# Kernel optimization log

Hardware: AMD Instinct MI355X
Metric: run time of the kernel (lower is better)

## Reference

```python
import jax, jax.numpy as jnp
import numpy as np

L, B, T, V, E, H = 6, 4, 1024, 32000, 768, 12
D = E // H  # head_size = 64


def setup_inputs() -> dict:
    key = jax.random.key(0)
    ks = jax.random.split(key, 12)
    s = 0.02
    n = lambda k, shape: jax.random.normal(k, shape, jnp.float32) * s
    return {
        "idx": jax.random.randint(ks[0], (B, T), 0, V),
        "tok_emb": n(ks[1], (V, E)),
        "pos_emb": n(ks[2], (T, E)),
        "ln1_w": jnp.ones((L, E)), "ln1_b": jnp.zeros((L, E)),
        "wq": n(ks[3], (L, E, H, D)),
        "wk": n(ks[4], (L, E, H, D)),
        "wv": n(ks[5], (L, E, H, D)),
        "wo": n(ks[6], (L, E, E)), "bo": jnp.zeros((L, E)),
        "ln2_w": jnp.ones((L, E)), "ln2_b": jnp.zeros((L, E)),
        "w1": n(ks[7], (L, E, 4 * E)), "b1": jnp.zeros((L, 4 * E)),
        "w2": n(ks[8], (L, 4 * E, E)), "b2": jnp.zeros((L, E)),
        "lnf_w": jnp.ones((E,)), "lnf_b": jnp.zeros((E,)),
        "head_w": n(ks[9], (E, V)), "head_b": jnp.zeros((V,)),
    }


def _ln(x, w, b, eps=1e-5):
    m = x.mean(-1, keepdims=True)
    v = ((x - m) ** 2).mean(-1, keepdims=True)
    return (x - m) * jax.lax.rsqrt(v + eps) * w + b


def _forward(idx, tok_emb, pos_emb, ln1_w, ln1_b, wq, wk, wv, wo, bo,
             ln2_w, ln2_b, w1, b1, w2, b2, lnf_w, lnf_b, head_w, head_b):
    t = idx.shape[1]
    x = tok_emb[idx] + pos_emb[None, :t]          # [B,T,E]
    causal = jnp.tril(jnp.ones((t, t), bool))     # tril buffer
    scale = jnp.asarray(D, x.dtype) ** -0.5       # k.shape[-1] ** -0.5

    def block(x, p):
        l1w, l1b, Wq, Wk, Wv, Wo, Bo, l2w, l2b, W1, B1, W2, B2 = p
        h = _ln(x, l1w, l1b)
        q = jnp.einsum('btc,chd->bthd', h, Wq)
        k = jnp.einsum('btc,chd->bthd', h, Wk)
        v = jnp.einsum('btc,chd->bthd', h, Wv)
        wei = jnp.einsum('bqhd,bkhd->bhqk', q, k) * scale
        wei = jnp.where(causal, wei, -jnp.inf)
        wei = jax.nn.softmax(wei, axis=-1)
        att = jnp.einsum('bhqk,bkhd->bqhd', wei, v).reshape(x.shape)
        x = x + (att @ Wo + Bo)
        h2 = _ln(x, l2w, l2b)
        x = x + (jax.nn.relu(h2 @ W1 + B1) @ W2 + B2)
        return x, None

    params = (ln1_w, ln1_b, wq, wk, wv, wo, bo, ln2_w, ln2_b, w1, b1, w2, b2)
    x, _ = jax.lax.scan(block, x, params)
    x = _ln(x, lnf_w, lnf_b)
    return x @ head_w + head_b                    # [B,T,V] logits


def reference(idx, tok_emb, pos_emb, ln1_w, ln1_b, wq, wk, wv, wo, bo,
              ln2_w, ln2_b, w1, b1, w2, b2, lnf_w, lnf_b, head_w, head_b):
    return _forward(idx, tok_emb, pos_emb, ln1_w, ln1_b, wq, wk, wv, wo, bo,
                    ln2_w, ln2_b, w1, b1, w2, b2, lnf_w, lnf_b, head_w, head_b)
```

## Files before the change

### kernel.cpp

```cpp
#include <hip/hip_runtime.h>
#include <hip/hip_bf16.h>
#include <math.h>

#define L_LAYERS 6
#define BB 4
#define TT 1024
#define VV 32000
#define EE 768
#define HH 12
#define DD 64
#define BT (BB * TT)

typedef unsigned short u16;
typedef unsigned int   u32;
typedef __attribute__((ext_vector_type(8))) short short8;
typedef __attribute__((ext_vector_type(8))) unsigned short ushort8v;
typedef __attribute__((ext_vector_type(4))) float f32x4;

__device__ __forceinline__ float b2f_lo(u32 u) { union { u32 i; float f; } c; c.i = u << 16;          return c.f; }
__device__ __forceinline__ float b2f_hi(u32 u) { union { u32 i; float f; } c; c.i = u & 0xffff0000u;  return c.f; }
__device__ __forceinline__ u16  f2b(float f)   { union { float f; u32 i; } c{f}; u32 r = c.i + 0x7fffu + ((c.i >> 16) & 1u); return (u16)(r >> 16); }

__device__ __forceinline__ void gload16(const void* g, void* l) {
    __builtin_amdgcn_global_load_lds(
        (const __attribute__((address_space(1))) void*)g,
        (__attribute__((address_space(3))) void*)l, 16, 0, 0);
}

__global__ __launch_bounds__(256) void embed_kernel(
    const int* __restrict__ idx, const float* __restrict__ tok_emb,
    const float* __restrict__ pos_emb, float* __restrict__ x)
{
    int i = blockIdx.x * 256 + threadIdx.x;
    int e  = i % EE;
    int bt = i / EE;
    int t  = bt % TT;
    int tok = idx[bt];
    x[i] = tok_emb[(size_t)tok * EE + e] + pos_emb[(size_t)t * EE + e];
}

__global__ __launch_bounds__(256) void ln_kernel(
    const float* __restrict__ X, const float* __restrict__ w,
    const float* __restrict__ b, u16* __restrict__ Y)
{
    const int tid = threadIdx.x;
    const size_t row = blockIdx.x;
    const float* x = X + row * EE;

    float v0 = x[tid], v1 = x[tid + 256], v2 = x[tid + 512];

    __shared__ float red[256];
    red[tid] = v0 + v1 + v2;
    __syncthreads();
    for (int off = 128; off > 0; off >>= 1) {
        if (tid < off) red[tid] += red[tid + off];
        __syncthreads();
    }
    float mean = red[0] * (1.0f / EE);
    __syncthreads();
    float d0 = v0 - mean, d1 = v1 - mean, d2 = v2 - mean;
    red[tid] = d0 * d0 + d1 * d1 + d2 * d2;
    __syncthreads();
    for (int off = 128; off > 0; off >>= 1) {
        if (tid < off) red[tid] += red[tid + off];
        __syncthreads();
    }
    float rstd = rsqrtf(red[0] * (1.0f / EE) + 1e-5f);

    u16* y = Y + row * EE;
    y[tid]       = f2b(d0 * rstd * w[tid]       + b[tid]);
    y[tid + 256] = f2b(d1 * rstd * w[tid + 256] + b[tid + 256]);
    y[tid + 512] = f2b(d2 * rstd * w[tid + 512] + b[tid + 512]);
}

__device__ __forceinline__ void transpose_tile(
    const float* __restrict__ W, u16* __restrict__ Wt,
    int K, int N, int kt, int nt)
{
    __shared__ float t[32][33];
    const int k0 = kt * 32;
    const int n0 = nt * 32;
    const int c = threadIdx.x & 31;
    const int r = threadIdx.x >> 5;
    #pragma unroll
    for (int i = 0; i < 4; i++)
        t[r + i * 8][c] = W[(size_t)(k0 + r + i * 8) * N + n0 + c];
    __syncthreads();
    #pragma unroll
    for (int i = 0; i < 4; i++) {
        int rr = r + i * 8;
        Wt[(size_t)(n0 + rr) * K + k0 + c] = f2b(t[c][rr]);
    }
}

__global__ __launch_bounds__(256) void transpose_cvt(
    const float* __restrict__ W, u16* __restrict__ Wt, int K, int N)
{
    transpose_tile(W, Wt, K, N, blockIdx.y, blockIdx.x);
}

__global__ __launch_bounds__(256) void transpose_layer(
    const float* __restrict__ wq, const float* __restrict__ wk,
    const float* __restrict__ wv, const float* __restrict__ wo,
    const float* __restrict__ w1, const float* __restrict__ w2,
    u16* __restrict__ wt)
{
    const int t = blockIdx.x;
    if (t < 2304) {
        const int m = t / 576, r = t % 576;
        const float* Ws[4] = {wq, wk, wv, wo};
        transpose_tile(Ws[m], wt + (size_t)m * 768 * 768, 768, 768, r / 24, r % 24);
    } else if (t < 4608) {
        const int r = t - 2304;
        transpose_tile(w1, wt + (size_t)4 * 768 * 768, 768, 3072, r / 96, r % 96);
    } else {
        const int r = t - 4608;
        transpose_tile(w2, wt + (size_t)4 * 768 * 768 + (size_t)3072 * 768,
                       3072, 768, r / 24, r % 24);
    }
}

template<int RELU, int RES, int OUTBF, int MFRAG>
__global__ __launch_bounds__(256) void gemm_bf16(
    const u16* __restrict__ A,
    const u16* __restrict__ Bt,
    const float* __restrict__ bias,
    const float* __restrict__ res,
    void* __restrict__ Cv,
    int M, int N, int K)
{
    constexpr int TM = MFRAG * 32;
    __shared__ u16 As[TM * 64];
    __shared__ u16 Bs[128 * 64];

    const int tid  = threadIdx.x;
    const int lane = tid & 63;
    const int w    = tid >> 6;
    const int wr   = w >> 1, wc = w & 1;
    const int m0 = blockIdx.x * TM;
    const int n0 = blockIdx.y * 128;

    const int cs = (lane & 7) ^ (lane >> 3);
    const int rl = lane >> 3;

    int aoff[2 * MFRAG], boff[8];
    const int kq = lane >> 4;
    #pragma unroll
    for (int mi = 0; mi < MFRAG; mi++) {
        int rg = wr * (MFRAG * 16) + mi * 16 + (lane & 15);
        #pragma unroll
        for (int ks = 0; ks < 2; ks++)
            aoff[2 * mi + ks] = rg * 64 + (((ks * 4 + kq) ^ (rg & 7)) * 8);
    }
    #pragma unroll
    for (int ni = 0; ni < 4; ni++) {
        int rg = wc * 64 + ni * 16 + (lane & 15);
        #pragma unroll
        for (int ks = 0; ks < 2; ks++)
            boff[2 * ni + ks] = rg * 64 + (((ks * 4 + kq) ^ (rg & 7)) * 8);
    }

    f32x4 acc[MFRAG][4] = {};

    for (int k0 = 0; k0 < K; k0 += 64) {
        __syncthreads();
        #pragma unroll
        for (int i = 0; i < MFRAG; i++) {
            const int seg = i * 4 + w;
            const int row = seg * 8 + rl;
            gload16(A + (size_t)(m0 + row) * K + k0 + cs * 8, &As[seg * 512]);
        }
        #pragma unroll
        for (int i = 0; i < 4; i++) {
            const int seg = i * 4 + w;
            const int row = seg * 8 + rl;
            gload16(Bt + (size_t)(n0 + row) * K + k0 + cs * 8, &Bs[seg * 512]);
        }
        __syncthreads();
        #pragma unroll
        for (int ks = 0; ks < 2; ks++) {
            short8 af[MFRAG], bfv[4];
            #pragma unroll
            for (int mi = 0; mi < MFRAG; mi++) af[mi] = *(const short8*)&As[aoff[2 * mi + ks]];
            #pragma unroll
            for (int ni = 0; ni < 4; ni++) bfv[ni] = *(const short8*)&Bs[boff[2 * ni + ks]];
            #pragma unroll
            for (int mi = 0; mi < MFRAG; mi++)
                #pragma unroll
                for (int ni = 0; ni < 4; ni++)
                    acc[mi][ni] = __builtin_amdgcn_mfma_f32_16x16x32_bf16(
                        af[mi], bfv[ni], acc[mi][ni], 0, 0, 0);
        }
    }

    const int rbase = m0 + wr * (MFRAG * 16) + (lane >> 4) * 4;
    const int cbase = n0 + wc * 64 + (lane & 15);
    #pragma unroll
    for (int ni = 0; ni < 4; ni++) {
        const int c = cbase + ni * 16;
        const float bv = bias ? bias[c] : 0.0f;
        #pragma unroll
        for (int mi = 0; mi < MFRAG; mi++) {
            const int r = rbase + mi * 16;
            #pragma unroll
            for (int i = 0; i < 4; i++) {
                float v = acc[mi][ni][i] + bv;
                const size_t off = (size_t)(r + i) * N + c;
                if (RES)  v += res[off];
                if (RELU) v = fmaxf(v, 0.0f);
                if (OUTBF) ((u16*)Cv)[off] = f2b(v);
                else       ((float*)Cv)[off] = v;
            }
        }
    }
}

#define AST 76
__global__ __launch_bounds__(256) void attn_mfma(
    const u16* __restrict__ qkv, u16* __restrict__ O)
{
    const int tid = threadIdx.x;
    const int qi = blockIdx.x;
    const int h  = blockIdx.y;
    const int b  = blockIdx.z;
    const int q0 = qi * 64;

    __shared__ u16 Ks[64 * AST];
    __shared__ u16 Vt[64 * AST];
    __shared__ u16 Ps[64 * AST];

    const int lane = tid & 63;
    const int w    = tid >> 6;
    const int lr   = lane & 15;
    const int lk   = lane >> 4;

    const int sr = tid >> 2;
    const int sc = tid & 3;

    {
        const u16* src = qkv + (size_t)(b * TT + q0 + sr) * 2304 + h * 64 + sc * 16;
        *(ushort8v*)&Ps[sr * AST + sc * 16]     = *(const ushort8v*)src;
        *(ushort8v*)&Ps[sr * AST + sc * 16 + 8] = *(const ushort8v*)(src + 8);
    }
    __syncthreads();
    short8 aq[2];
    #pragma unroll
    for (int ks = 0; ks < 2; ks++)
        aq[ks] = *(const short8*)&Ps[(w * 16 + lr) * AST + lk * 8 + ks * 32];

    f32x4 oacc[4] = {};
    float m_run[4], l_run[4];
    #pragma unroll
    for (int i = 0; i < 4; i++) { m_run[i] = -3.0e38f; l_run[i] = 0.0f; }

    const int qrow = q0 + w * 16 + lk * 4;
    const int ntile = qi + 1;

    for (int t = 0; t < ntile; t++) {
        const int k0 = t * 64;
        __syncthreads();
        {
            const u16* ksrc = qkv + (size_t)(b * TT + k0 + sr) * 2304 + 768 + h * 64 + sc * 16;
            *(ushort8v*)&Ks[sr * AST + sc * 16]     = *(const ushort8v*)ksrc;
            *(ushort8v*)&Ks[sr * AST + sc * 16 + 8] = *(const ushort8v*)(ksrc + 8);
            const u16* vsrc = ksrc + 768;
            ushort8v v0 = *(const ushort8v*)vsrc;
            ushort8v v1 = *(const ushort8v*)(vsrc + 8);
            #pragma unroll
            for (int j = 0; j < 8; j++) Vt[(sc * 16 + j) * AST + sr]     = v0[j];
            #pragma unroll
            for (int j = 0; j < 8; j++) Vt[(sc * 16 + 8 + j) * AST + sr] = v1[j];
        }
        __syncthreads();

        f32x4 sfrag[4] = {};
        #pragma unroll
        for (int ks = 0; ks < 2; ks++)
            #pragma unroll
            for (int nt = 0; nt < 4; nt++) {
                short8 bk = *(const short8*)&Ks[(nt * 16 + lr) * AST + lk * 8 + ks * 32];
                sfrag[nt] = __builtin_amdgcn_mfma_f32_16x16x32_bf16(aq[ks], bk, sfrag[nt], 0, 0, 0);
            }

        float sv[4][4];
        #pragma unroll
        for (int i = 0; i < 4; i++) {
            float mx = -3.0e38f;
            #pragma unroll
            for (int nt = 0; nt < 4; nt++) {
                float s = sfrag[nt][i] * 0.125f;
                if (t == qi && (k0 + nt * 16 + lr) > (qrow + i)) s = -3.0e38f;
                sv[i][nt] = s;
                mx = fmaxf(mx, s);
            }
            mx = fmaxf(mx, __shfl_xor(mx, 1));
            mx = fmaxf(mx, __shfl_xor(mx, 2));
            mx = fmaxf(mx, __shfl_xor(mx, 4));
            mx = fmaxf(mx, __shfl_xor(mx, 8));
            const float m_new = fmaxf(m_run[i], mx);
            const float scale = __expf(m_run[i] - m_new);
            float rs = 0.0f;
            #pragma unroll
            for (int nt = 0; nt < 4; nt++) {
                float p = __expf(sv[i][nt] - m_new);
                sv[i][nt] = p;
                rs += p;
            }
            rs += __shfl_xor(rs, 1);
            rs += __shfl_xor(rs, 2);
            rs += __shfl_xor(rs, 4);
            rs += __shfl_xor(rs, 8);
            l_run[i] = l_run[i] * scale + rs;
            m_run[i] = m_new;
            #pragma unroll
            for (int dt = 0; dt < 4; dt++) oacc[dt][i] *= scale;
        }

        #pragma unroll
        for (int i = 0; i < 4; i++)
            #pragma unroll
            for (int nt = 0; nt < 4; nt++)
                Ps[(w * 16 + lk * 4 + i) * AST + nt * 16 + lr] = f2b(sv[i][nt]);
        __syncthreads();

        #pragma unroll
        for (int ks = 0; ks < 2; ks++) {
            short8 ap = *(const short8*)&Ps[(w * 16 + lr) * AST + lk * 8 + ks * 32];
            #pragma unroll
            for (int dt = 0; dt < 4; dt++) {
                short8 bv = *(const short8*)&Vt[(dt * 16 + lr) * AST + lk * 8 + ks * 32];
                oacc[dt] = __builtin_amdgcn_mfma_f32_16x16x32_bf16(ap, bv, oacc[dt], 0, 0, 0);
            }
        }
    }

    #pragma unroll
    for (int i = 0; i < 4; i++) {
        const float inv = 1.0f / l_run[i];
        u16* dst = O + (size_t)(b * TT + q0 + w * 16 + lk * 4 + i) * 768 + h * 64 + lr;
        #pragma unroll
        for (int dt = 0; dt < 4; dt++)
            dst[dt * 16] = f2b(oacc[dt][i] * inv);
    }
}

extern "C" void kernel_launch(void* const* d_in, const int* in_sizes, int n_in,
                              void* d_out, int out_size, void* d_ws, size_t ws_size,
                              hipStream_t stream)
{
    (void)in_sizes; (void)n_in; (void)out_size; (void)ws_size;

    const int*   idx     = (const int*)  d_in[0];
    const float* tok_emb = (const float*)d_in[1];
    const float* pos_emb = (const float*)d_in[2];
    const float* ln1_w   = (const float*)d_in[3];
    const float* ln1_b   = (const float*)d_in[4];
    const float* wq      = (const float*)d_in[5];
    const float* wk      = (const float*)d_in[6];
    const float* wv      = (const float*)d_in[7];
    const float* wo      = (const float*)d_in[8];
    const float* bo      = (const float*)d_in[9];
    const float* ln2_w   = (const float*)d_in[10];
    const float* ln2_b   = (const float*)d_in[11];
    const float* w1      = (const float*)d_in[12];
    const float* b1      = (const float*)d_in[13];
    const float* w2      = (const float*)d_in[14];
    const float* b2      = (const float*)d_in[15];
    const float* lnf_w   = (const float*)d_in[16];
    const float* lnf_b   = (const float*)d_in[17];
    const float* head_w  = (const float*)d_in[18];
    const float* head_b  = (const float*)d_in[19];
    float* out = (float*)d_out;

    const size_t S = (size_t)BT * EE;
    float* x   = (float*)d_ws;
    u16*  qkv  = (u16*)(x + S);
    u16*  hb   = qkv + (size_t)BT * 2304;
    u16*  ffh  = hb + S;
    u16*  wt   = ffh + (size_t)BT * 3072;

    embed_kernel<<<BT * EE / 256, 256, 0, stream>>>(idx, tok_emb, pos_emb, x);

    for (int l = 0; l < L_LAYERS; l++) {
        const size_t oE  = (size_t)l * EE;
        const size_t oEE = (size_t)l * EE * EE;
        const size_t oEF = (size_t)l * EE * 4 * EE;

        transpose_layer<<<6912, 256, 0, stream>>>(
            wq + oEE, wk + oEE, wv + oEE, wo + oEE, w1 + oEF, w2 + oEF, wt);

        ln_kernel<<<BT, 256, 0, stream>>>(x, ln1_w + oE, ln1_b + oE, hb);
        gemm_bf16<0, 0, 1, 4><<<dim3(BT / 128, 2304 / 128), 256, 0, stream>>>(
            hb, wt, nullptr, nullptr, qkv, BT, 2304, 768);
        attn_mfma<<<dim3(TT / 64, HH, BB), 256, 0, stream>>>(qkv, hb);
        gemm_bf16<0, 1, 0, 2><<<dim3(BT / 64, 768 / 128), 256, 0, stream>>>(
            hb, wt + (size_t)3 * 768 * 768, bo + oE, x, x, BT, 768, 768);
        ln_kernel<<<BT, 256, 0, stream>>>(x, ln2_w + oE, ln2_b + oE, hb);
        gemm_bf16<1, 0, 1, 4><<<dim3(BT / 128, 3072 / 128), 256, 0, stream>>>(
            hb, wt + (size_t)4 * 768 * 768, b1 + (size_t)l * 4 * EE, nullptr, ffh, BT, 3072, 768);
        gemm_bf16<0, 1, 0, 2><<<dim3(BT / 64, 768 / 128), 256, 0, stream>>>(
            ffh, wt + (size_t)4 * 768 * 768 + (size_t)3072 * 768, b2 + oE, x, x, BT, 768, 3072);
    }

    ln_kernel<<<BT, 256, 0, stream>>>(x, lnf_w, lnf_b, hb);
    transpose_cvt<<<dim3(VV / 32, EE / 32), 256, 0, stream>>>(head_w, wt, EE, VV);
    gemm_bf16<0, 0, 0, 4><<<dim3(BT / 128, VV / 128), 256, 0, stream>>>(
        hb, wt, head_b, nullptr, out, BT, VV, 768);
}
```

Before: 1.567 ms.

## Add 256x256 double-buffered GEMM kernel for QKV, FFN1 and LM head

Adds a new 512-thread GEMM with 256x256 output tiles, double-buffered LDS staging through direct global-to-LDS loads, and an XCD-aware block remap. It replaces the 128x128 kernel for the QKV, FFN-up and vocabulary-head projections. The larger tiles raise arithmetic intensity and reuse per block, and prefetching two stages ahead hides load latency. In exchange the kernel uses 128 KB of LDS and many accumulator registers per block, which lowers occupancy, and the small QKV grid of 144 blocks may underfill the GPU.

```diff
diff --git a/kernel.cpp b/kernel.cpp
--- a/kernel.cpp
+++ b/kernel.cpp
@@ -122,12 +122,9 @@
 
 template<int RELU, int RES, int OUTBF, int MFRAG>
 __global__ __launch_bounds__(256) void gemm_bf16(
-    const u16* __restrict__ A,
-    const u16* __restrict__ Bt,
-    const float* __restrict__ bias,
-    const float* __restrict__ res,
-    void* __restrict__ Cv,
-    int M, int N, int K)
+    const u16* __restrict__ A, const u16* __restrict__ Bt,
+    const float* __restrict__ bias, const float* __restrict__ res,
+    void* __restrict__ Cv, int M, int N, int K)
 {
     constexpr int TM = MFRAG * 32;
     __shared__ u16 As[TM * 64];
@@ -208,6 +205,130 @@
                 const size_t off = (size_t)(r + i) * N + c;
                 if (RES)  v += res[off];
                 if (RELU) v = fmaxf(v, 0.0f);
+                if (OUTBF) ((u16*)Cv)[off] = f2b(v);
+                else       ((float*)Cv)[off] = v;
+            }
+        }
+    }
+}
+
+template<int RELU, int OUTBF>
+__global__ __launch_bounds__(512, 2) void gemm256(
+    const u16* __restrict__ A, const u16* __restrict__ Bt,
+    const float* __restrict__ bias, void* __restrict__ Cv,
+    int M, int N, int K)
+{
+    __shared__ u16 SA[2][256 * 64];
+    __shared__ u16 SB[2][256 * 64];
+
+    const int tid  = threadIdx.x;
+    const int lane = tid & 63;
+    const int w    = tid >> 6;
+    const int wr   = w >> 2, wc = w & 3;
+
+    const int gx  = gridDim.x;
+    const int nwg = gx * gridDim.y;
+    const int lin = blockIdx.y * gx + blockIdx.x;
+    const int q8  = nwg >> 3;
+    const int s   = (lin & 7) * q8 + (lin >> 3);
+    const int m0  = (s % gx) * 256;
+    const int n0  = (s / gx) * 256;
+
+    const int cs = (lane & 7) ^ (lane >> 3);
+    const int rl = lane >> 3;
+
+    const int lr = lane & 15, kq = lane >> 4;
+    int aoff[16], boff[8];
+    #pragma unroll
+    for (int mi = 0; mi < 8; mi++) {
+        int rg = wr * 128 + mi * 16 + lr;
+        #pragma unroll
+        for (int ks = 0; ks < 2; ks++)
+            aoff[2 * mi + ks] = rg * 64 + (((ks * 4 + kq) ^ (rg & 7)) * 8);
+    }
+    #pragma unroll
+    for (int ni = 0; ni < 4; ni++) {
+        int rg = wc * 64 + ni * 16 + lr;
+        #pragma unroll
+        for (int ks = 0; ks < 2; ks++)
+            boff[2 * ni + ks] = rg * 64 + (((ks * 4 + kq) ^ (rg & 7)) * 8);
+    }
+
+    const int nt = K >> 6;
+
+    auto STAGE = [&](int t, int bf) {
+        const int k0 = t * 64;
+        #pragma unroll
+        for (int i = 0; i < 4; i++) {
+            const int seg = i * 8 + w;
+            const int row = seg * 8 + rl;
+            gload16(A + (size_t)(m0 + row) * K + k0 + cs * 8, &SA[bf][seg * 512]);
+        }
+        #pragma unroll
+        for (int i = 0; i < 4; i++) {
+            const int seg = i * 8 + w;
+            const int row = seg * 8 + rl;
+            gload16(Bt + (size_t)(n0 + row) * K + k0 + cs * 8, &SB[bf][seg * 512]);
+        }
+    };
+
+    f32x4 acc[8][4] = {};
+
+    STAGE(0, 0);
+    STAGE(1, 1);
+    asm volatile("s_waitcnt vmcnt(8)" ::: "memory");
+    __builtin_amdgcn_s_barrier();
+    __builtin_amdgcn_sched_barrier(0);
+
+    for (int t = 0; t < nt; t++) {
+        const int cur = t & 1;
+        __builtin_amdgcn_s_setprio(1);
+        #pragma unroll
+        for (int ks = 0; ks < 2; ks++) {
+            short8 af[8], bv[4];
+            #pragma unroll
+            for (int mi = 0; mi < 8; mi++) af[mi] = *(const short8*)&SA[cur][aoff[2 * mi + ks]];
+            #pragma unroll
+            for (int ni = 0; ni < 4; ni++) bv[ni] = *(const short8*)&SB[cur][boff[2 * ni + ks]];
+            #pragma unroll
+            for (int mi = 0; mi < 8; mi++)
+                #pragma unroll
+                for (int ni = 0; ni < 4; ni++)
+                    acc[mi][ni] = __builtin_amdgcn_mfma_f32_16x16x32_bf16(
+                        af[mi], bv[ni], acc[mi][ni], 0, 0, 0);
+        }
+        __builtin_amdgcn_s_setprio(0);
+
+        if (t < nt - 1) {
+            __builtin_amdgcn_sched_barrier(0);
+            __builtin_amdgcn_s_barrier();
+            __builtin_amdgcn_sched_barrier(0);
+            if (t + 2 < nt) {
+                STAGE(t + 2, cur);
+                asm volatile("s_waitcnt vmcnt(8)" ::: "memory");
+            } else {
+                asm volatile("s_waitcnt vmcnt(0)" ::: "memory");
+            }
+            __builtin_amdgcn_sched_barrier(0);
+            __builtin_amdgcn_s_barrier();
+            __builtin_amdgcn_sched_barrier(0);
+        }
+    }
+
+    const int rbase = m0 + wr * 128 + (lane >> 4) * 4;
+    const int cbase = n0 + wc * 64 + lr;
+    #pragma unroll
+    for (int ni = 0; ni < 4; ni++) {
+        const int c = cbase + ni * 16;
+        const float bvf = bias ? bias[c] : 0.0f;
+        #pragma unroll
+        for (int mi = 0; mi < 8; mi++) {
+            const int r = rbase + mi * 16;
+            #pragma unroll
+            for (int i = 0; i < 4; i++) {
+                float v = acc[mi][ni][i] + bvf;
+                if (RELU) v = fmaxf(v, 0.0f);
+                const size_t off = (size_t)(r + i) * N + c;
                 if (OUTBF) ((u16*)Cv)[off] = f2b(v);
                 else       ((float*)Cv)[off] = v;
             }
@@ -390,20 +511,20 @@
             wq + oEE, wk + oEE, wv + oEE, wo + oEE, w1 + oEF, w2 + oEF, wt);
 
         ln_kernel<<<BT, 256, 0, stream>>>(x, ln1_w + oE, ln1_b + oE, hb);
-        gemm_bf16<0, 0, 1, 4><<<dim3(BT / 128, 2304 / 128), 256, 0, stream>>>(
-            hb, wt, nullptr, nullptr, qkv, BT, 2304, 768);
+        gemm256<0, 1><<<dim3(BT / 256, 2304 / 256), 512, 0, stream>>>(
+            hb, wt, nullptr, qkv, BT, 2304, 768);
         attn_mfma<<<dim3(TT / 64, HH, BB), 256, 0, stream>>>(qkv, hb);
         gemm_bf16<0, 1, 0, 2><<<dim3(BT / 64, 768 / 128), 256, 0, stream>>>(
             hb, wt + (size_t)3 * 768 * 768, bo + oE, x, x, BT, 768, 768);
         ln_kernel<<<BT, 256, 0, stream>>>(x, ln2_w + oE, ln2_b + oE, hb);
-        gemm_bf16<1, 0, 1, 4><<<dim3(BT / 128, 3072 / 128), 256, 0, stream>>>(
-            hb, wt + (size_t)4 * 768 * 768, b1 + (size_t)l * 4 * EE, nullptr, ffh, BT, 3072, 768);
+        gemm256<1, 1><<<dim3(BT / 256, 3072 / 256), 512, 0, stream>>>(
+            hb, wt + (size_t)4 * 768 * 768, b1 + (size_t)l * 4 * EE, ffh, BT, 3072, 768);
         gemm_bf16<0, 1, 0, 2><<<dim3(BT / 64, 768 / 128), 256, 0, stream>>>(
             ffh, wt + (size_t)4 * 768 * 768 + (size_t)3072 * 768, b2 + oE, x, x, BT, 768, 3072);
     }
 
     ln_kernel<<<BT, 256, 0, stream>>>(x, lnf_w, lnf_b, hb);
     transpose_cvt<<<dim3(VV / 32, EE / 32), 256, 0, stream>>>(head_w, wt, EE, VV);
-    gemm_bf16<0, 0, 0, 4><<<dim3(BT / 128, VV / 128), 256, 0, stream>>>(
-        hb, wt, head_b, nullptr, out, BT, VV, 768);
-}
+    gemm256<0, 0><<<dim3(BT / 256, VV / 256), 512, 0, stream>>>(
+        hb, wt, head_b, out, BT, VV, 768);
+}
```

New measurement: 1.687 ms. 1.08x slower.

## Double-buffer attention K/V tiles, skip softmax rescale, vectorize LM-head stores

Applied to the files above, without the earlier changes.

Attention now double-buffers K (async global-to-LDS loads with a swizzled layout) and V (register-staged, transposed as packed pairs). The next tile's loads are issued during the current tile's compute, which removes one barrier per iteration. The online softmax skips rescaling unless any row's max grows by more than 8, a lazy-rescale trick that relies on fp32 headroom. The LM-head GEMM stages its output tile through shared memory so it can write coalesced 16-byte float4 stores instead of scattered scalar ones, at the cost of extra barriers and LDS traffic.

```diff
diff --git a/kernel.cpp b/kernel.cpp
--- a/kernel.cpp
+++ b/kernel.cpp
@@ -120,18 +120,16 @@
     }
 }
 
-template<int RELU, int RES, int OUTBF, int MFRAG>
+template<int RELU, int RES, int OUTBF, int MFRAG, int VECST>
 __global__ __launch_bounds__(256) void gemm_bf16(
-    const u16* __restrict__ A,
-    const u16* __restrict__ Bt,
-    const float* __restrict__ bias,
-    const float* __restrict__ res,
-    void* __restrict__ Cv,
-    int M, int N, int K)
+    const u16* __restrict__ A, const u16* __restrict__ Bt,
+    const float* __restrict__ bias, const float* __restrict__ res,
+    void* __restrict__ Cv, int M, int N, int K)
 {
     constexpr int TM = MFRAG * 32;
-    __shared__ u16 As[TM * 64];
-    __shared__ u16 Bs[128 * 64];
+    __shared__ u16 SH[(TM + 128) * 64];
+    u16* As = SH;
+    u16* Bs = SH + TM * 64;
 
     const int tid  = threadIdx.x;
     const int lane = tid & 63;
@@ -195,27 +193,59 @@
 
     const int rbase = m0 + wr * (MFRAG * 16) + (lane >> 4) * 4;
     const int cbase = n0 + wc * 64 + (lane & 15);
-    #pragma unroll
-    for (int ni = 0; ni < 4; ni++) {
-        const int c = cbase + ni * 16;
-        const float bv = bias ? bias[c] : 0.0f;
-        #pragma unroll
-        for (int mi = 0; mi < MFRAG; mi++) {
-            const int r = rbase + mi * 16;
-            #pragma unroll
-            for (int i = 0; i < 4; i++) {
-                float v = acc[mi][ni][i] + bv;
-                const size_t off = (size_t)(r + i) * N + c;
-                if (RES)  v += res[off];
-                if (RELU) v = fmaxf(v, 0.0f);
-                if (OUTBF) ((u16*)Cv)[off] = f2b(v);
-                else       ((float*)Cv)[off] = v;
-            }
-        }
-    }
-}
-
-#define AST 76
+
+    if (VECST) {
+        __syncthreads();
+        float* CF = (float*)SH;
+        #pragma unroll
+        for (int ch = 0; ch < 2; ++ch) {
+            if (wr == ch) {
+                #pragma unroll
+                for (int ni = 0; ni < 4; ni++) {
+                    const int c = cbase + ni * 16;
+                    const float bvf = bias ? bias[c] : 0.0f;
+                    #pragma unroll
+                    for (int mi = 0; mi < MFRAG; mi++)
+                        #pragma unroll
+                        for (int i = 0; i < 4; i++)
+                            CF[(mi * 16 + kq * 4 + i) * 128 + wc * 64 + ni * 16 + (lane & 15)]
+                                = acc[mi][ni][i] + bvf;
+                }
+            }
+            __syncthreads();
+            const int rr = tid >> 5;
+            const int cc = (tid & 31) * 4;
+            #pragma unroll
+            for (int j = 0; j < 8; ++j) {
+                const int r = rr + j * 8;
+                *(f32x4*)&((float*)Cv)[(size_t)(m0 + ch * 64 + r) * N + n0 + cc]
+                    = *(const f32x4*)&CF[r * 128 + cc];
+            }
+            if (ch == 0) __syncthreads();
+        }
+    } else {
+        #pragma unroll
+        for (int ni = 0; ni < 4; ni++) {
+            const int c = cbase + ni * 16;
+            const float bv = bias ? bias[c] : 0.0f;
+            #pragma unroll
+            for (int mi = 0; mi < MFRAG; mi++) {
+                const int r = rbase + mi * 16;
+                #pragma unroll
+                for (int i = 0; i < 4; i++) {
+                    float v = acc[mi][ni][i] + bv;
+                    const size_t off = (size_t)(r + i) * N + c;
+                    if (RES)  v += res[off];
+                    if (RELU) v = fmaxf(v, 0.0f);
+                    if (OUTBF) ((u16*)Cv)[off] = f2b(v);
+                    else       ((float*)Cv)[off] = v;
+                }
+            }
+        }
+    }
+}
+
+#define AST 72
 __global__ __launch_bounds__(256) void attn_mfma(
     const u16* __restrict__ qkv, u16* __restrict__ O)
 {
@@ -225,8 +255,8 @@
     const int b  = blockIdx.z;
     const int q0 = qi * 64;
 
-    __shared__ u16 Ks[64 * AST];
-    __shared__ u16 Vt[64 * AST];
+    __shared__ u16 Ks[2][64 * 64];
+    __shared__ u16 Vt[2][64 * AST];
     __shared__ u16 Ps[64 * AST];
 
     const int lane = tid & 63;
@@ -234,10 +264,13 @@
     const int lr   = lane & 15;
     const int lk   = lane >> 4;
 
-    const int sr = tid >> 2;
-    const int sc = tid & 3;
+    const int cs = (lane & 7) ^ (lane >> 3);
+    const int rl = lane >> 3;
+    const int vk2 = tid & 31;
+    const int vdc = tid >> 5;
 
     {
+        const int sr = tid >> 2, sc = tid & 3;
         const u16* src = qkv + (size_t)(b * TT + q0 + sr) * 2304 + h * 64 + sc * 16;
         *(ushort8v*)&Ps[sr * AST + sc * 16]     = *(const ushort8v*)src;
         *(ushort8v*)&Ps[sr * AST + sc * 16 + 8] = *(const ushort8v*)(src + 8);
@@ -248,41 +281,61 @@
     for (int ks = 0; ks < 2; ks++)
         aq[ks] = *(const short8*)&Ps[(w * 16 + lr) * AST + lk * 8 + ks * 32];
 
+    ushort8v vr0, vr1;
+    auto K_ISSUE = [&](int t, int bf) {
+        const int k0 = t * 64;
+        #pragma unroll
+        for (int j = 0; j < 2; ++j) {
+            const int seg = j * 4 + w;
+            const int row = seg * 8 + rl;
+            gload16(qkv + (size_t)(b * TT + k0 + row) * 2304 + 768 + h * 64 + cs * 8,
+                    &Ks[bf][seg * 512]);
+        }
+    };
+    auto V_LOAD = [&](int t) {
+        const int k0 = t * 64;
+        const u16* p = qkv + (size_t)(b * TT + k0 + 2 * vk2) * 2304 + 1536 + h * 64 + vdc * 8;
+        vr0 = *(const ushort8v*)p;
+        vr1 = *(const ushort8v*)(p + 2304);
+    };
+    auto V_WRITE = [&](int bf) {
+        #pragma unroll
+        for (int j = 0; j < 8; ++j) {
+            const u32 val = (u32)vr0[j] | ((u32)vr1[j] << 16);
+            *(u32*)&Vt[bf][(vdc * 8 + j) * AST + 2 * vk2] = val;
+        }
+    };
+
+    K_ISSUE(0, 0);
+    V_LOAD(0);
+    V_WRITE(0);
+    __syncthreads();
+
     f32x4 oacc[4] = {};
     float m_run[4], l_run[4];
     #pragma unroll
     for (int i = 0; i < 4; i++) { m_run[i] = -3.0e38f; l_run[i] = 0.0f; }
 
     const int qrow = q0 + w * 16 + lk * 4;
-    const int ntile = qi + 1;
-
-    for (int t = 0; t < ntile; t++) {
+
+    for (int t = 0; t <= qi; ++t) {
+        const int cur = t & 1;
+
+        f32x4 sfrag[4] = {};
+        #pragma unroll
+        for (int ks = 0; ks < 2; ks++)
+            #pragma unroll
+            for (int nt = 0; nt < 4; nt++) {
+                const int rg = nt * 16 + lr;
+                short8 bk = *(const short8*)&Ks[cur][rg * 64 + (((ks * 4 + lk) ^ (rg & 7)) * 8)];
+                sfrag[nt] = __builtin_amdgcn_mfma_f32_16x16x32_bf16(aq[ks], bk, sfrag[nt], 0, 0, 0);
+            }
+
+        if (t < qi) { K_ISSUE(t + 1, cur ^ 1); V_LOAD(t + 1); }
+
         const int k0 = t * 64;
-        __syncthreads();
-        {
-            const u16* ksrc = qkv + (size_t)(b * TT + k0 + sr) * 2304 + 768 + h * 64 + sc * 16;
-            *(ushort8v*)&Ks[sr * AST + sc * 16]     = *(const ushort8v*)ksrc;
-            *(ushort8v*)&Ks[sr * AST + sc * 16 + 8] = *(const ushort8v*)(ksrc + 8);
-            const u16* vsrc = ksrc + 768;
-            ushort8v v0 = *(const ushort8v*)vsrc;
-            ushort8v v1 = *(const ushort8v*)(vsrc + 8);
-            #pragma unroll
-            for (int j = 0; j < 8; j++) Vt[(sc * 16 + j) * AST + sr]     = v0[j];
-            #pragma unroll
-            for (int j = 0; j < 8; j++) Vt[(sc * 16 + 8 + j) * AST + sr] = v1[j];
-        }
-        __syncthreads();
-
-        f32x4 sfrag[4] = {};
-        #pragma unroll
-        for (int ks = 0; ks < 2; ks++)
-            #pragma unroll
-            for (int nt = 0; nt < 4; nt++) {
-                short8 bk = *(const short8*)&Ks[(nt * 16 + lr) * AST + lk * 8 + ks * 32];
-                sfrag[nt] = __builtin_amdgcn_mfma_f32_16x16x32_bf16(aq[ks], bk, sfrag[nt], 0, 0, 0);
-            }
-
-        float sv[4][4];
+        float sv[4][4], mxv[4];
+        float need = 0.0f;
         #pragma unroll
         for (int i = 0; i < 4; i++) {
             float mx = -3.0e38f;
@@ -297,12 +350,26 @@
             mx = fmaxf(mx, __shfl_xor(mx, 2));
             mx = fmaxf(mx, __shfl_xor(mx, 4));
             mx = fmaxf(mx, __shfl_xor(mx, 8));
-            const float m_new = fmaxf(m_run[i], mx);
-            const float scale = __expf(m_run[i] - m_new);
+            mxv[i] = mx;
+            need = fmaxf(need, mx - m_run[i]);
+        }
+        if (!__all(need <= 8.0f)) {
+            #pragma unroll
+            for (int i = 0; i < 4; i++) {
+                const float m_new = fmaxf(m_run[i], mxv[i]);
+                const float scale = __expf(m_run[i] - m_new);
+                l_run[i] *= scale;
+                #pragma unroll
+                for (int dt = 0; dt < 4; dt++) oacc[dt][i] *= scale;
+                m_run[i] = m_new;
+            }
+        }
+        #pragma unroll
+        for (int i = 0; i < 4; i++) {
             float rs = 0.0f;
             #pragma unroll
             for (int nt = 0; nt < 4; nt++) {
-                float p = __expf(sv[i][nt] - m_new);
+                const float p = __expf(sv[i][nt] - m_run[i]);
                 sv[i][nt] = p;
                 rs += p;
             }
@@ -310,10 +377,7 @@
             rs += __shfl_xor(rs, 2);
             rs += __shfl_xor(rs, 4);
             rs += __shfl_xor(rs, 8);
-            l_run[i] = l_run[i] * scale + rs;
-            m_run[i] = m_new;
-            #pragma unroll
-            for (int dt = 0; dt < 4; dt++) oacc[dt][i] *= scale;
+            l_run[i] += rs;
         }
 
         #pragma unroll
@@ -321,17 +385,19 @@
             #pragma unroll
             for (int nt = 0; nt < 4; nt++)
                 Ps[(w * 16 + lk * 4 + i) * AST + nt * 16 + lr] = f2b(sv[i][nt]);
-        __syncthreads();
 
         #pragma unroll
         for (int ks = 0; ks < 2; ks++) {
             short8 ap = *(const short8*)&Ps[(w * 16 + lr) * AST + lk * 8 + ks * 32];
             #pragma unroll
             for (int dt = 0; dt < 4; dt++) {
-                short8 bv = *(const short8*)&Vt[(dt * 16 + lr) * AST + lk * 8 + ks * 32];
+                short8 bv = *(const short8*)&Vt[cur][(dt * 16 + lr) * AST + lk * 8 + ks * 32];
                 oacc[dt] = __builtin_amdgcn_mfma_f32_16x16x32_bf16(ap, bv, oacc[dt], 0, 0, 0);
             }
         }
+
+        if (t < qi) V_WRITE(cur ^ 1);
+        __syncthreads();
     }
 
     #pragma unroll
@@ -390,20 +456,20 @@
             wq + oEE, wk + oEE, wv + oEE, wo + oEE, w1 + oEF, w2 + oEF, wt);
 
         ln_kernel<<<BT, 256, 0, stream>>>(x, ln1_w + oE, ln1_b + oE, hb);
-        gemm_bf16<0, 0, 1, 4><<<dim3(BT / 128, 2304 / 128), 256, 0, stream>>>(
+        gemm_bf16<0, 0, 1, 4, 0><<<dim3(BT / 128, 2304 / 128), 256, 0, stream>>>(
             hb, wt, nullptr, nullptr, qkv, BT, 2304, 768);
         attn_mfma<<<dim3(TT / 64, HH, BB), 256, 0, stream>>>(qkv, hb);
-        gemm_bf16<0, 1, 0, 2><<<dim3(BT / 64, 768 / 128), 256, 0, stream>>>(
+        gemm_bf16<0, 1, 0, 2, 0><<<dim3(BT / 64, 768 / 128), 256, 0, stream>>>(
             hb, wt + (size_t)3 * 768 * 768, bo + oE, x, x, BT, 768, 768);
         ln_kernel<<<BT, 256, 0, stream>>>(x, ln2_w + oE, ln2_b + oE, hb);
-        gemm_bf16<1, 0, 1, 4><<<dim3(BT / 128, 3072 / 128), 256, 0, stream>>>(
+        gemm_bf16<1, 0, 1, 4, 0><<<dim3(BT / 128, 3072 / 128), 256, 0, stream>>>(
             hb, wt + (size_t)4 * 768 * 768, b1 + (size_t)l * 4 * EE, nullptr, ffh, BT, 3072, 768);
-        gemm_bf16<0, 1, 0, 2><<<dim3(BT / 64, 768 / 128), 256, 0, stream>>>(
+        gemm_bf16<0, 1, 0, 2, 0><<<dim3(BT / 64, 768 / 128), 256, 0, stream>>>(
             ffh, wt + (size_t)4 * 768 * 768 + (size_t)3072 * 768, b2 + oE, x, x, BT, 768, 3072);
     }
 
     ln_kernel<<<BT, 256, 0, stream>>>(x, lnf_w, lnf_b, hb);
     transpose_cvt<<<dim3(VV / 32, EE / 32), 256, 0, stream>>>(head_w, wt, EE, VV);
-    gemm_bf16<0, 0, 0, 4><<<dim3(BT / 128, VV / 128), 256, 0, stream>>>(
+    gemm_bf16<0, 0, 0, 4, 1><<<dim3(BT / 128, VV / 128), 256, 0, stream>>>(
         hb, wt, head_b, nullptr, out, BT, VV, 768);
 }
```

After: 1.532 ms. 2.2% less time.
